# Optimization experiments

Measured on AMD Instinct MI355X. Metric: run time of the kernel, lower is better.

Reference implementation:

```python
import jax, jax.numpy as jnp
import numpy as np
import math

SQRT2 = float(np.sqrt(2.0))
INV_SQRT_2PI = float(1.0 / np.sqrt(2.0 * np.pi))


def _trunc_prob(x, mu, sigma):
    # Faithful port of TruncNormal.prob with a=-10, b=10
    a, b = -10.0, 10.0
    phi_b = 0.5 * (1.0 + jax.scipy.special.erf((b - mu) / sigma / SQRT2))
    phi_a = 0.5 * (1.0 + jax.scipy.special.erf((a - mu) / sigma / SQRT2))
    xs = jnp.where(x > b, x + 100.0, x)
    xs = jnp.where(xs < a, xs - 100.0, xs)
    xn = (xs - mu) / sigma
    dens = jnp.exp(-0.5 * xn * xn) * INV_SQRT_2PI
    dens = jnp.where((xn > b) | (xn < a), 0.0, dens)
    return dens / (phi_b - phi_a) + 1e-10


def _S_single(zg, tt, Wx, bx, Wt, bt, Wt2, bt2, Wf, bf, Wo, bo):
    # One tiny MLP applied to one group-slice zg (shape [g]) at scalar time tt.
    g = Wx.shape[0]
    x = jnp.tanh(Wx @ zg + bx)
    half = g // 2
    freqs = jnp.exp(jnp.arange(half, dtype=zg.dtype) * (-math.log(10000.0) / half))
    te = tt * freqs
    temb = jnp.concatenate([jnp.sin(te), jnp.cos(te)])  # [g]
    tv = jax.nn.gelu(Wt @ temb + bt, approximate=False)  # torch nn.GELU (exact)
    tv = Wt2 @ tv + bt2
    h = jnp.tanh(Wf @ (x + tv) + bf)
    return jnp.tanh(Wo @ h + bo)[0]  # scalar S


def _derivs(zg, tt, Wx, bx, Wt, bt, Wt2, bt2, Wf, bf, Wo, bo):
    p = (Wx, bx, Wt, bt, Wt2, bt2, Wf, bf, Wo, bo)
    f = lambda z_, t_: _S_single(z_, t_, *p)
    S = f(zg, tt)
    s_z = jax.grad(f, 0)(zg, tt)                    # dS/dz         [g]
    H = jax.jacfwd(jax.grad(f, 0), 0)(zg, tt)       # H[j,k]=d2S/dzj dzk  [g,g]
    dSdt = jax.grad(f, 1)(zg, tt)                   # dS/dt scalar
    return S, s_z, H, dSdt


def reference(z, time_step, mu, sigma, Wx, bx, Wt, bt, Wt2, bt2, Wf, bf, Wo, bo, beta):
    G, g = Wx.shape[0], Wx.shape[1]
    B = z.shape[0]
    tt = time_step[0]

    sig2 = sigma ** 2 + 1e-5
    nlp = -(z - mu) / sig2                                   # nabla_log_phi [B,n_in]
    dlp = -1.0 / sig2                                        # delta_log_phi (scalar-ish)
    dpp = ((z - mu) ** 2 - sigma ** 2) / (sigma ** 4 + 1e-5)  # delta_phi_over_phi
    rho = _trunc_prob(z, mu, sigma)

    to_g = lambda a: a.reshape(B, G, g).transpose(1, 0, 2)   # [G,B,g]
    zr, nlp_r, dpp_r, rho_r = to_g(z), to_g(nlp), to_g(dpp), to_g(rho)

    over_b = jax.vmap(_derivs, in_axes=(0, None) + (None,) * 10)
    over_g = jax.vmap(over_b, in_axes=(0, None) + (0,) * 10)
    S, s_z, H, dSdt = over_g(zr, tt, Wx, bx, Wt, bt, Wt2, bt2, Wf, bf, Wo, bo)
    # S [G,B], s_z [G,B,g], H [G,B,g,g], dSdt [G,B]

    bb = beta.reshape(G, 1, 1)
    u = S[..., None] - bb * jnp.log(jnp.prod(rho_r, axis=2, keepdims=True))  # [G,B,1]
    u_z = s_z - bb * nlp_r                                                    # [G,B,g]
    # torch grad(S.sum(), t): t is a single shared (1,1) tensor -> gradient sums over batch
    dSdt_sum = dSdt.sum(axis=1).reshape(G, 1, 1)
    # grad((rho*u_z).sum(), z_temp): rho and nabla_log_phi are constants wrt z_temp,
    # so gradient = sum_j rho_j * H[j,k]
    corr = jnp.einsum('gbj,gbjk->gbk', rho_r, H)
    u_t = dSdt_sum + bb * corr / (rho_r + 1e-5)
    # grad(s_z.sum(), z_temp)[k] = sum_j H[j,k]
    u_zz = H.sum(axis=2) - bb * dlp
    pde = u_t + 0.5 * u_z ** 2 + 0.125 * bb ** 2 * (nlp_r ** 2 - 2.0 * dpp_r)

    to_bn = lambda a: a.transpose(1, 0, 2).reshape(B, -1)
    return to_bn(pde), to_bn(u_z), u[:, :, 0].transpose(1, 0), to_bn(u_zz)


def setup_inputs() -> dict:
    B, N_IN, g = 8192, 512, 4
    G = N_IN // g
    key = jax.random.key(0)
    ks = jax.random.split(key, 16)

    def lin_w(k, fo, fi):
        return (jax.random.normal(k, (G, fo, fi), jnp.float32) / np.sqrt(fi)).astype(jnp.float32)

    def lin_b(k, fo):
        return (0.01 * jax.random.normal(k, (G, fo), jnp.float32)).astype(jnp.float32)

    return {
        "z": jax.random.normal(ks[0], (B, N_IN), jnp.float32),
        "time_step": jnp.ones((1,), jnp.float32),
        "mu": jnp.zeros((1,), jnp.float32),
        "sigma": jnp.ones((1,), jnp.float32),
        "Wx": lin_w(ks[1], g, g), "bx": lin_b(ks[2], g),
        "Wt": lin_w(ks[3], g, g), "bt": lin_b(ks[4], g),
        "Wt2": lin_w(ks[5], g, g), "bt2": lin_b(ks[6], g),
        "Wf": lin_w(ks[7], g, g), "bf": lin_b(ks[8], g),
        "Wo": lin_w(ks[9], 1, g), "bo": lin_b(ks[10], 1),
        "beta": jnp.ones((G, 1), jnp.float32),
    }
```

## Files before the change

### kernel.cpp

```cpp
#include <hip/hip_runtime.h>
#include <math.h>

#define NG 128
#define NIN 512
#define OFF1 4194304
#define OFF2 8388608
#define OFF3 9437184

#define INV_SQRT_2PI 0.3989422804014327f
#define INV_SQRT2    0.7071067811865476f

__device__ __forceinline__ float ftanh(float x){
    float e = __expf(2.0f*x);
    float r = __builtin_amdgcn_rcpf(e + 1.0f);
    return 1.0f - 2.0f*r;
}
__device__ __forceinline__ float frcp(float x){ return __builtin_amdgcn_rcpf(x); }

__device__ __forceinline__ float gelu_f(float x){
    return 0.5f*x*(1.0f + erff(x*INV_SQRT2));
}
__device__ __forceinline__ float gelu_df(float x){
    return 0.5f*(1.0f + erff(x*INV_SQRT2)) + x*INV_SQRT_2PI*expf(-0.5f*x*x);
}

__global__ void k_pre(const float* __restrict__ ts,
                      const float* __restrict__ mup, const float* __restrict__ sigp,
                      const float* __restrict__ Wt,  const float* __restrict__ bt,
                      const float* __restrict__ Wt2, const float* __restrict__ bt2,
                      float* __restrict__ tv_ws, float* __restrict__ dtv_ws,
                      float* __restrict__ consts){
    int g = threadIdx.x;
    if (g == 0){
        float mu = mup[0], sigma = sigp[0];
        float sig2   = sigma*sigma + 1e-5f;
        float phi_b  = 0.5f*(1.0f+erff((10.0f-mu)/sigma*INV_SQRT2));
        float phi_a  = 0.5f*(1.0f+erff((-10.0f-mu)/sigma*INV_SQRT2));
        consts[0] = sig2;
        consts[1] = -1.0f/sig2;
        consts[2] = 1.0f/(sigma*sigma*sigma*sigma + 1e-5f);
        consts[3] = 1.0f/(phi_b-phi_a);
        consts[4] = mu;
        consts[5] = 1.0f/sigma;
        consts[6] = sigma;
    }
    if (g >= NG) return;
    float t  = ts[0];
    float f1 = expf(-0.5f*logf(10000.0f));
    float te0 = t, te1 = t*f1;
    float temb[4]  = { sinf(te0),  sinf(te1),     cosf(te0),     cosf(te1) };
    float dtemb[4] = { cosf(te0),  f1*cosf(te1), -sinf(te0), -f1*sinf(te1) };
    float tg[4], dg[4];
    #pragma unroll
    for (int i=0;i<4;i++){
        float a = bt[g*4+i], d = 0.0f;
        #pragma unroll
        for (int j=0;j<4;j++){
            float w = Wt[g*16+i*4+j];
            a += w*temb[j]; d += w*dtemb[j];
        }
        tg[i] = gelu_f(a);
        dg[i] = gelu_df(a)*d;
    }
    #pragma unroll
    for (int j=0;j<4;j++){
        float a = bt2[g*4+j], d = 0.0f;
        #pragma unroll
        for (int i=0;i<4;i++){
            float w = Wt2[g*16+j*4+i];
            a += w*tg[i]; d += w*dg[i];
        }
        tv_ws[g*4+j]  = a;
        dtv_ws[g*4+j] = d;
    }
}

__global__ __launch_bounds__(256) void k_dsdt(const float* __restrict__ z,
    const float* __restrict__ Wx, const float* __restrict__ bx,
    const float* __restrict__ Wf, const float* __restrict__ bf,
    const float* __restrict__ Wo, const float* __restrict__ bo,
    const float* __restrict__ tv_ws, const float* __restrict__ dtv_ws,
    float* __restrict__ partial){
    const int tid  = threadIdx.x;
    const int gidx = tid & 127;
    const int lb   = tid >> 7;
    float wx[16], wf[16];
    #pragma unroll
    for (int i=0;i<4;i++){
        float4 a4 = ((const float4*)(Wx + gidx*16))[i];
        wx[i*4+0]=a4.x; wx[i*4+1]=a4.y; wx[i*4+2]=a4.z; wx[i*4+3]=a4.w;
        float4 b4 = ((const float4*)(Wf + gidx*16))[i];
        wf[i*4+0]=b4.x; wf[i*4+1]=b4.y; wf[i*4+2]=b4.z; wf[i*4+3]=b4.w;
    }
    float4 t4;
    t4 = ((const float4*)bx)[gidx];     float bxA[4]={t4.x,t4.y,t4.z,t4.w};
    t4 = ((const float4*)bf)[gidx];     float bfA[4]={t4.x,t4.y,t4.z,t4.w};
    t4 = ((const float4*)Wo)[gidx];     float w3[4] ={t4.x,t4.y,t4.z,t4.w};
    t4 = ((const float4*)tv_ws)[gidx];  float tvA[4]={t4.x,t4.y,t4.z,t4.w};
    t4 = ((const float4*)dtv_ws)[gidx]; float dtvA[4]={t4.x,t4.y,t4.z,t4.w};
    float bo0 = bo[gidx];

    float acc = 0.0f;
    const int b0 = blockIdx.x*4 + lb;
    #pragma unroll
    for (int k=0;k<2;k++){
        int b = b0 + 2*k;
        float4 zv = *((const float4*)(z + b*NIN + gidx*4));
        float zz[4]={zv.x,zv.y,zv.z,zv.w};
        float u1[4];
        #pragma unroll
        for (int i=0;i<4;i++){
            float a = bxA[i] + wx[i*4]*zz[0]+wx[i*4+1]*zz[1]+wx[i*4+2]*zz[2]+wx[i*4+3]*zz[3];
            u1[i] = ftanh(a) + tvA[i];
        }
        float hp[4];
        float a3 = bo0;
        #pragma unroll
        for (int i=0;i<4;i++){
            float a = bfA[i] + wf[i*4]*u1[0]+wf[i*4+1]*u1[1]+wf[i*4+2]*u1[2]+wf[i*4+3]*u1[3];
            float h = ftanh(a);
            hp[i] = 1.0f - h*h;
            a3 += w3[i]*h;
        }
        float S = ftanh(a3), sp = 1.0f - S*S;
        float q[4]={0.f,0.f,0.f,0.f};
        #pragma unroll
        for (int i=0;i<4;i++){
            float vi = sp*w3[i]*hp[i];
            #pragma unroll
            for (int j=0;j<4;j++) q[j] += vi*wf[i*4+j];
        }
        acc += q[0]*dtvA[0]+q[1]*dtvA[1]+q[2]*dtvA[2]+q[3]*dtvA[3];
    }
    __shared__ float sred[256];
    sred[tid] = acc;
    __syncthreads();
    if (tid < 128) partial[blockIdx.x*128 + tid] = sred[tid] + sred[tid+128];
}

__global__ __launch_bounds__(256) void k_red(const float* __restrict__ partial,
                                             float* __restrict__ dsum){
    int g = blockIdx.x;
    int tid = threadIdx.x;
    float a = 0.0f;
    for (int i=tid;i<2048;i+=256) a += partial[i*128+g];
    __shared__ float s[256];
    s[tid] = a;
    __syncthreads();
    if (tid < 64){
        a = s[tid] + s[tid+64] + s[tid+128] + s[tid+192];
        #pragma unroll
        for (int o=32;o>0;o>>=1) a += __shfl_down(a, o);
        if (tid==0) dsum[g] = a;
    }
}

__global__ __launch_bounds__(256) void k_main(const float* __restrict__ z,
    const float* __restrict__ Wx, const float* __restrict__ bx,
    const float* __restrict__ Wf, const float* __restrict__ bf,
    const float* __restrict__ Wo, const float* __restrict__ bo,
    const float* __restrict__ betap, const float* __restrict__ tv_ws,
    const float* __restrict__ consts,
    const float* __restrict__ dsum, float* __restrict__ out){
    const int tid  = threadIdx.x;
    const int gidx = tid & 127;
    const int b    = blockIdx.x*2 + (tid>>7);

    const float sig2    = consts[0];
    const float dlp     = consts[1];
    const float inv_s4  = consts[2];
    const float invZ    = consts[3];
    const float mu      = consts[4];
    const float inv_sig = consts[5];
    const float sigma   = consts[6];
    const float inv_sig2 = frcp(sig2);

    float wx[16], wf[16];
    #pragma unroll
    for (int i=0;i<4;i++){
        float4 a4 = ((const float4*)(Wx + gidx*16))[i];
        wx[i*4+0]=a4.x; wx[i*4+1]=a4.y; wx[i*4+2]=a4.z; wx[i*4+3]=a4.w;
        float4 b4 = ((const float4*)(Wf + gidx*16))[i];
        wf[i*4+0]=b4.x; wf[i*4+1]=b4.y; wf[i*4+2]=b4.z; wf[i*4+3]=b4.w;
    }
    float4 t4;
    t4 = ((const float4*)bx)[gidx];    float bxA[4]={t4.x,t4.y,t4.z,t4.w};
    t4 = ((const float4*)bf)[gidx];    float bfA[4]={t4.x,t4.y,t4.z,t4.w};
    t4 = ((const float4*)Wo)[gidx];    float w3[4] ={t4.x,t4.y,t4.z,t4.w};
    t4 = ((const float4*)tv_ws)[gidx]; float tvA[4]={t4.x,t4.y,t4.z,t4.w};
    const float bo0    = bo[gidx];
    const float bb     = betap[gidx];
    const float dS_sum = dsum[gidx];

    float4 zv = *((const float4*)(z + b*NIN + gidx*4));
    float zz[4]={zv.x,zv.y,zv.z,zv.w};

    float x[4], xp[4], u1[4];
    #pragma unroll
    for (int i=0;i<4;i++){
        float a = bxA[i] + wx[i*4]*zz[0]+wx[i*4+1]*zz[1]+wx[i*4+2]*zz[2]+wx[i*4+3]*zz[3];
        x[i] = ftanh(a); xp[i] = 1.0f - x[i]*x[i];
        u1[i] = x[i] + tvA[i];
    }
    float h[4], hp[4];
    float a3 = bo0;
    #pragma unroll
    for (int i=0;i<4;i++){
        float a = bfA[i] + wf[i*4]*u1[0]+wf[i*4+1]*u1[1]+wf[i*4+2]*u1[2]+wf[i*4+3]*u1[3];
        h[i] = ftanh(a); hp[i] = 1.0f - h[i]*h[i];
        a3 += w3[i]*h[i];
    }
    float S = ftanh(a3), sp = 1.0f - S*S;

    float Bm[16];
    #pragma unroll
    for (int i=0;i<4;i++){
        #pragma unroll
        for (int n=0;n<4;n++){
            float s = 0.0f;
            #pragma unroll
            for (int k=0;k<4;k++) s += wf[i*4+k]*xp[k]*wx[k*4+n];
            Bm[i*4+n]=s;
        }
    }
    float w3hp[4], v[4];
    #pragma unroll
    for (int i=0;i<4;i++){ w3hp[i]=w3[i]*hp[i]; v[i]=sp*w3hp[i]; }
    float q[4]={0.f,0.f,0.f,0.f};
    #pragma unroll
    for (int i=0;i<4;i++){
        #pragma unroll
        for (int j=0;j<4;j++) q[j] += v[i]*wf[i*4+j];
    }
    float c[4];
    #pragma unroll
    for (int n=0;n<4;n++){
        float s=0.0f;
        #pragma unroll
        for (int i=0;i<4;i++) s += w3hp[i]*Bm[i*4+n];
        c[n]=s;
    }
    const float alpha = -2.0f*S*sp;
    float bet[4], gam[4];
    #pragma unroll
    for (int i=0;i<4;i++){ bet[i] = -2.0f*h[i]*v[i]; gam[i] = -2.0f*x[i]*xp[i]*q[i]; }

    float rho[4], nlp[4], dpp[4];
    #pragma unroll
    for (int j=0;j<4;j++){
        float zj = zz[j];
        float xs = zj > 10.0f ? zj+100.0f : zj;
        xs = xs < -10.0f ? xs-100.0f : xs;
        float xn = (xs-mu)*inv_sig;
        float dens = __expf(-0.5f*xn*xn)*INV_SQRT_2PI;
        dens = (xn > 10.0f || xn < -10.0f) ? 0.0f : dens;
        rho[j] = dens*invZ + 1e-10f;
        nlp[j] = -(zj-mu)*inv_sig2;
        float d = zj-mu;
        dpp[j] = (d*d - sigma*sigma)*inv_s4;
    }
    float u_val = S - bb*__logf(rho[0]*rho[1]*rho[2]*rho[3]);

    float rc=0.0f, scs=0.0f;
    #pragma unroll
    for (int j=0;j<4;j++){ rc += rho[j]*c[j]; scs += c[j]; }
    float rB[4], sB[4], rA[4], sA[4];
    #pragma unroll
    for (int i=0;i<4;i++){
        float r=0.0f, s=0.0f, r2=0.0f, s2=0.0f;
        #pragma unroll
        for (int j=0;j<4;j++){
            r  += rho[j]*Bm[i*4+j]; s  += Bm[i*4+j];
            r2 += rho[j]*wx[i*4+j]; s2 += wx[i*4+j];
        }
        rB[i]=r; sB[i]=s; rA[i]=r2; sA[i]=s2;
    }

    float pde[4], uz[4], uzz[4];
    #pragma unroll
    for (int k=0;k<4;k++){
        float corr = alpha*rc*c[k];
        float hsum = alpha*scs*c[k];
        #pragma unroll
        for (int i=0;i<4;i++){
            corr += bet[i]*rB[i]*Bm[i*4+k];
            hsum += bet[i]*sB[i]*Bm[i*4+k];
            corr += gam[i]*rA[i]*wx[i*4+k];
            hsum += gam[i]*sA[i]*wx[i*4+k];
        }
        float uzk = sp*c[k] - bb*nlp[k];
        float utk = dS_sum + bb*corr*frcp(rho[k]+1e-5f);
        uz[k]  = uzk;
        uzz[k] = hsum - bb*dlp;
        pde[k] = utk + 0.5f*uzk*uzk + 0.125f*bb*bb*(nlp[k]*nlp[k] - 2.0f*dpp[k]);
    }

    const int base = b*NIN + gidx*4;
    *((float4*)(out + base))        = make_float4(pde[0],pde[1],pde[2],pde[3]);
    *((float4*)(out + OFF1 + base)) = make_float4(uz[0],uz[1],uz[2],uz[3]);
    out[OFF2 + b*NG + gidx] = u_val;
    *((float4*)(out + OFF3 + base)) = make_float4(uzz[0],uzz[1],uzz[2],uzz[3]);
}

extern "C" void kernel_launch(void* const* d_in, const int* in_sizes, int n_in,
                              void* d_out, int out_size, void* d_ws, size_t ws_size,
                              hipStream_t stream){
    (void)in_sizes; (void)n_in; (void)out_size; (void)ws_size;
    const float* z     = (const float*)d_in[0];
    const float* ts    = (const float*)d_in[1];
    const float* mu    = (const float*)d_in[2];
    const float* sigma = (const float*)d_in[3];
    const float* Wx    = (const float*)d_in[4];
    const float* bx    = (const float*)d_in[5];
    const float* Wt    = (const float*)d_in[6];
    const float* bt    = (const float*)d_in[7];
    const float* Wt2   = (const float*)d_in[8];
    const float* bt2   = (const float*)d_in[9];
    const float* Wf    = (const float*)d_in[10];
    const float* bf    = (const float*)d_in[11];
    const float* Wo    = (const float*)d_in[12];
    const float* bo    = (const float*)d_in[13];
    const float* beta  = (const float*)d_in[14];
    float* out = (float*)d_out;

    float* ws      = (float*)d_ws;
    float* tv_ws   = ws;
    float* dtv_ws  = ws + 512;
    float* consts  = ws + 1024;
    float* dsum    = ws + 1032;
    float* partial = ws + 1160;

    k_pre <<<1,   128, 0, stream>>>(ts, mu, sigma, Wt, bt, Wt2, bt2, tv_ws, dtv_ws, consts);
    k_dsdt<<<2048,256, 0, stream>>>(z, Wx, bx, Wf, bf, Wo, bo, tv_ws, dtv_ws, partial);
    k_red <<<128, 256, 0, stream>>>(partial, dsum);
    k_main<<<4096,256, 0, stream>>>(z, Wx, bx, Wf, bf, Wo, bo, beta, tv_ws, consts, dsum, out);
}
```

Baseline: 131.0 us.

## Fuse dS/dt partial sums into main kernel and add deferred pde fixup pass

Merges the time-embedding precompute, the dS/dt partial-reduction kernel and the main derivative kernel into one pass. Each thread now computes the forward pass and derivatives once per row, and the pde output is written without the global dS/dt sum. A small fixup kernel then adds the reduced per-group sum into the pde region. This removes the duplicated forward-pass compute and the second read of z, at the cost of an extra read-modify-write over the pde output and per-block recomputation of the constants and time-embedding MLP.

```diff
diff --git a/kernel.cpp b/kernel.cpp
--- a/kernel.cpp
+++ b/kernel.cpp
@@ -21,69 +21,33 @@
     return 0.5f*x*(1.0f + erff(x*INV_SQRT2));
 }
 __device__ __forceinline__ float gelu_df(float x){
-    return 0.5f*(1.0f + erff(x*INV_SQRT2)) + x*INV_SQRT_2PI*expf(-0.5f*x*x);
-}
-
-__global__ void k_pre(const float* __restrict__ ts,
-                      const float* __restrict__ mup, const float* __restrict__ sigp,
-                      const float* __restrict__ Wt,  const float* __restrict__ bt,
-                      const float* __restrict__ Wt2, const float* __restrict__ bt2,
-                      float* __restrict__ tv_ws, float* __restrict__ dtv_ws,
-                      float* __restrict__ consts){
-    int g = threadIdx.x;
-    if (g == 0){
-        float mu = mup[0], sigma = sigp[0];
-        float sig2   = sigma*sigma + 1e-5f;
-        float phi_b  = 0.5f*(1.0f+erff((10.0f-mu)/sigma*INV_SQRT2));
-        float phi_a  = 0.5f*(1.0f+erff((-10.0f-mu)/sigma*INV_SQRT2));
-        consts[0] = sig2;
-        consts[1] = -1.0f/sig2;
-        consts[2] = 1.0f/(sigma*sigma*sigma*sigma + 1e-5f);
-        consts[3] = 1.0f/(phi_b-phi_a);
-        consts[4] = mu;
-        consts[5] = 1.0f/sigma;
-        consts[6] = sigma;
-    }
-    if (g >= NG) return;
-    float t  = ts[0];
-    float f1 = expf(-0.5f*logf(10000.0f));
-    float te0 = t, te1 = t*f1;
-    float temb[4]  = { sinf(te0),  sinf(te1),     cosf(te0),     cosf(te1) };
-    float dtemb[4] = { cosf(te0),  f1*cosf(te1), -sinf(te0), -f1*sinf(te1) };
-    float tg[4], dg[4];
-    #pragma unroll
-    for (int i=0;i<4;i++){
-        float a = bt[g*4+i], d = 0.0f;
-        #pragma unroll
-        for (int j=0;j<4;j++){
-            float w = Wt[g*16+i*4+j];
-            a += w*temb[j]; d += w*dtemb[j];
-        }
-        tg[i] = gelu_f(a);
-        dg[i] = gelu_df(a)*d;
-    }
-    #pragma unroll
-    for (int j=0;j<4;j++){
-        float a = bt2[g*4+j], d = 0.0f;
-        #pragma unroll
-        for (int i=0;i<4;i++){
-            float w = Wt2[g*16+j*4+i];
-            a += w*tg[i]; d += w*dg[i];
-        }
-        tv_ws[g*4+j]  = a;
-        dtv_ws[g*4+j] = d;
-    }
-}
-
-__global__ __launch_bounds__(256) void k_dsdt(const float* __restrict__ z,
+    return 0.5f*(1.0f + erff(x*INV_SQRT2)) + x*INV_SQRT_2PI*__expf(-0.5f*x*x);
+}
+
+__global__ __launch_bounds__(256) void k_fused(const float* __restrict__ z,
+    const float* __restrict__ ts,
+    const float* __restrict__ mup, const float* __restrict__ sigp,
     const float* __restrict__ Wx, const float* __restrict__ bx,
+    const float* __restrict__ Wt, const float* __restrict__ bt,
+    const float* __restrict__ Wt2, const float* __restrict__ bt2,
     const float* __restrict__ Wf, const float* __restrict__ bf,
     const float* __restrict__ Wo, const float* __restrict__ bo,
-    const float* __restrict__ tv_ws, const float* __restrict__ dtv_ws,
-    float* __restrict__ partial){
+    const float* __restrict__ betap,
+    float* __restrict__ partial, float* __restrict__ out){
     const int tid  = threadIdx.x;
     const int gidx = tid & 127;
     const int lb   = tid >> 7;
+
+    const float mu = mup[0], sigma = sigp[0];
+    const float sig2     = sigma*sigma + 1e-5f;
+    const float inv_sig2 = frcp(sig2);
+    const float dlp      = -inv_sig2;
+    const float inv_s4   = frcp(sigma*sigma*sigma*sigma + 1e-5f);
+    const float inv_sig  = frcp(sigma);
+    const float phi_b    = 0.5f*(1.0f+erff((10.0f-mu)*inv_sig*INV_SQRT2));
+    const float phi_a    = 0.5f*(1.0f+erff((-10.0f-mu)*inv_sig*INV_SQRT2));
+    const float invZ     = frcp(phi_b-phi_a);
+
     float wx[16], wf[16];
     #pragma unroll
     for (int i=0;i<4;i++){
@@ -93,47 +57,166 @@
         wf[i*4+0]=b4.x; wf[i*4+1]=b4.y; wf[i*4+2]=b4.z; wf[i*4+3]=b4.w;
     }
     float4 t4;
-    t4 = ((const float4*)bx)[gidx];     float bxA[4]={t4.x,t4.y,t4.z,t4.w};
-    t4 = ((const float4*)bf)[gidx];     float bfA[4]={t4.x,t4.y,t4.z,t4.w};
-    t4 = ((const float4*)Wo)[gidx];     float w3[4] ={t4.x,t4.y,t4.z,t4.w};
-    t4 = ((const float4*)tv_ws)[gidx];  float tvA[4]={t4.x,t4.y,t4.z,t4.w};
-    t4 = ((const float4*)dtv_ws)[gidx]; float dtvA[4]={t4.x,t4.y,t4.z,t4.w};
-    float bo0 = bo[gidx];
-
-    float acc = 0.0f;
-    const int b0 = blockIdx.x*4 + lb;
-    #pragma unroll
-    for (int k=0;k<2;k++){
-        int b = b0 + 2*k;
+    t4 = ((const float4*)bx)[gidx];    float bxA[4]={t4.x,t4.y,t4.z,t4.w};
+    t4 = ((const float4*)bf)[gidx];    float bfA[4]={t4.x,t4.y,t4.z,t4.w};
+    t4 = ((const float4*)Wo)[gidx];    float w3[4] ={t4.x,t4.y,t4.z,t4.w};
+    const float bo0 = bo[gidx];
+    const float bb  = betap[gidx];
+
+    float tvA[4], dtvA[4];
+    {
+        const float t  = ts[0];
+        const float f1 = 0.01f;
+        float te0 = t, te1 = t*f1;
+        float s0, c0, s1, c1;
+        __sincosf(te0, &s0, &c0);
+        __sincosf(te1, &s1, &c1);
+        float temb[4]  = { s0, s1, c0, c1 };
+        float dtemb[4] = { c0, f1*c1, -s0, -f1*s1 };
+        float tg[4], dg[4];
+        #pragma unroll
+        for (int i=0;i<4;i++){
+            float a = bt[gidx*4+i], d = 0.0f;
+            #pragma unroll
+            for (int j=0;j<4;j++){
+                float w = Wt[gidx*16+i*4+j];
+                a += w*temb[j]; d += w*dtemb[j];
+            }
+            tg[i] = gelu_f(a);
+            dg[i] = gelu_df(a)*d;
+        }
+        #pragma unroll
+        for (int j=0;j<4;j++){
+            float a = bt2[gidx*4+j], d = 0.0f;
+            #pragma unroll
+            for (int i=0;i<4;i++){
+                float w = Wt2[gidx*16+j*4+i];
+                a += w*tg[i]; d += w*dg[i];
+            }
+            tvA[j]  = a;
+            dtvA[j] = d;
+        }
+    }
+
+    float dsdt_acc = 0.0f;
+    const int b_base = blockIdx.x*4 + lb*2;
+
+    for (int r=0;r<2;r++){
+        const int b = b_base + r;
         float4 zv = *((const float4*)(z + b*NIN + gidx*4));
         float zz[4]={zv.x,zv.y,zv.z,zv.w};
-        float u1[4];
+
+        float x[4], xp[4], u1[4];
         #pragma unroll
         for (int i=0;i<4;i++){
             float a = bxA[i] + wx[i*4]*zz[0]+wx[i*4+1]*zz[1]+wx[i*4+2]*zz[2]+wx[i*4+3]*zz[3];
-            u1[i] = ftanh(a) + tvA[i];
-        }
-        float hp[4];
+            x[i] = ftanh(a); xp[i] = 1.0f - x[i]*x[i];
+            u1[i] = x[i] + tvA[i];
+        }
+        float h[4], hp[4];
         float a3 = bo0;
         #pragma unroll
         for (int i=0;i<4;i++){
             float a = bfA[i] + wf[i*4]*u1[0]+wf[i*4+1]*u1[1]+wf[i*4+2]*u1[2]+wf[i*4+3]*u1[3];
-            float h = ftanh(a);
-            hp[i] = 1.0f - h*h;
-            a3 += w3[i]*h;
+            h[i] = ftanh(a); hp[i] = 1.0f - h[i]*h[i];
+            a3 += w3[i]*h[i];
         }
         float S = ftanh(a3), sp = 1.0f - S*S;
+
+        float Bm[16];
+        #pragma unroll
+        for (int i=0;i<4;i++){
+            #pragma unroll
+            for (int n=0;n<4;n++){
+                float s = 0.0f;
+                #pragma unroll
+                for (int k=0;k<4;k++) s += wf[i*4+k]*xp[k]*wx[k*4+n];
+                Bm[i*4+n]=s;
+            }
+        }
+        float w3hp[4], v[4];
+        #pragma unroll
+        for (int i=0;i<4;i++){ w3hp[i]=w3[i]*hp[i]; v[i]=sp*w3hp[i]; }
         float q[4]={0.f,0.f,0.f,0.f};
         #pragma unroll
         for (int i=0;i<4;i++){
-            float vi = sp*w3[i]*hp[i];
-            #pragma unroll
-            for (int j=0;j<4;j++) q[j] += vi*wf[i*4+j];
-        }
-        acc += q[0]*dtvA[0]+q[1]*dtvA[1]+q[2]*dtvA[2]+q[3]*dtvA[3];
-    }
+            #pragma unroll
+            for (int j=0;j<4;j++) q[j] += v[i]*wf[i*4+j];
+        }
+        dsdt_acc += q[0]*dtvA[0]+q[1]*dtvA[1]+q[2]*dtvA[2]+q[3]*dtvA[3];
+
+        float c[4];
+        #pragma unroll
+        for (int n=0;n<4;n++){
+            float s=0.0f;
+            #pragma unroll
+            for (int i=0;i<4;i++) s += w3hp[i]*Bm[i*4+n];
+            c[n]=s;
+        }
+        const float alpha = -2.0f*S*sp;
+        float bet[4], gam[4];
+        #pragma unroll
+        for (int i=0;i<4;i++){ bet[i] = -2.0f*h[i]*v[i]; gam[i] = -2.0f*x[i]*xp[i]*q[i]; }
+
+        float rho[4], nlp[4], dpp[4];
+        #pragma unroll
+        for (int j=0;j<4;j++){
+            float zj = zz[j];
+            float xs = zj > 10.0f ? zj+100.0f : zj;
+            xs = xs < -10.0f ? xs-100.0f : xs;
+            float xn = (xs-mu)*inv_sig;
+            float dens = __expf(-0.5f*xn*xn)*INV_SQRT_2PI;
+            dens = (xn > 10.0f || xn < -10.0f) ? 0.0f : dens;
+            rho[j] = dens*invZ + 1e-10f;
+            nlp[j] = -(zj-mu)*inv_sig2;
+            float d = zj-mu;
+            dpp[j] = (d*d - sigma*sigma)*inv_s4;
+        }
+        float u_val = S - bb*__logf(rho[0]*rho[1]*rho[2]*rho[3]);
+
+        float rc=0.0f, scs=0.0f;
+        #pragma unroll
+        for (int j=0;j<4;j++){ rc += rho[j]*c[j]; scs += c[j]; }
+        float rB[4], sB[4], rA[4], sA[4];
+        #pragma unroll
+        for (int i=0;i<4;i++){
+            float r1=0.0f, s=0.0f, r2=0.0f, s2=0.0f;
+            #pragma unroll
+            for (int j=0;j<4;j++){
+                r1 += rho[j]*Bm[i*4+j]; s  += Bm[i*4+j];
+                r2 += rho[j]*wx[i*4+j]; s2 += wx[i*4+j];
+            }
+            rB[i]=r1; sB[i]=s; rA[i]=r2; sA[i]=s2;
+        }
+
+        float pde[4], uz[4], uzz[4];
+        #pragma unroll
+        for (int k=0;k<4;k++){
+            float corr = alpha*rc*c[k];
+            float hsum = alpha*scs*c[k];
+            #pragma unroll
+            for (int i=0;i<4;i++){
+                corr += bet[i]*rB[i]*Bm[i*4+k];
+                hsum += bet[i]*sB[i]*Bm[i*4+k];
+                corr += gam[i]*rA[i]*wx[i*4+k];
+                hsum += gam[i]*sA[i]*wx[i*4+k];
+            }
+            float uzk = sp*c[k] - bb*nlp[k];
+            uz[k]  = uzk;
+            uzz[k] = hsum - bb*dlp;
+            pde[k] = bb*corr*frcp(rho[k]+1e-5f)
+                   + 0.5f*uzk*uzk + 0.125f*bb*bb*(nlp[k]*nlp[k] - 2.0f*dpp[k]);
+        }
+
+        const int base = b*NIN + gidx*4;
+        *((float4*)(out + base))        = make_float4(pde[0],pde[1],pde[2],pde[3]);
+        *((float4*)(out + OFF1 + base)) = make_float4(uz[0],uz[1],uz[2],uz[3]);
+        out[OFF2 + b*NG + gidx] = u_val;
+        *((float4*)(out + OFF3 + base)) = make_float4(uzz[0],uzz[1],uzz[2],uzz[3]);
+    }
+
     __shared__ float sred[256];
-    sred[tid] = acc;
+    sred[tid] = dsdt_acc;
     __syncthreads();
     if (tid < 128) partial[blockIdx.x*128 + tid] = sred[tid] + sred[tid+128];
 }
@@ -155,151 +238,14 @@
     }
 }
 
-__global__ __launch_bounds__(256) void k_main(const float* __restrict__ z,
-    const float* __restrict__ Wx, const float* __restrict__ bx,
-    const float* __restrict__ Wf, const float* __restrict__ bf,
-    const float* __restrict__ Wo, const float* __restrict__ bo,
-    const float* __restrict__ betap, const float* __restrict__ tv_ws,
-    const float* __restrict__ consts,
-    const float* __restrict__ dsum, float* __restrict__ out){
-    const int tid  = threadIdx.x;
-    const int gidx = tid & 127;
-    const int b    = blockIdx.x*2 + (tid>>7);
-
-    const float sig2    = consts[0];
-    const float dlp     = consts[1];
-    const float inv_s4  = consts[2];
-    const float invZ    = consts[3];
-    const float mu      = consts[4];
-    const float inv_sig = consts[5];
-    const float sigma   = consts[6];
-    const float inv_sig2 = frcp(sig2);
-
-    float wx[16], wf[16];
-    #pragma unroll
-    for (int i=0;i<4;i++){
-        float4 a4 = ((const float4*)(Wx + gidx*16))[i];
-        wx[i*4+0]=a4.x; wx[i*4+1]=a4.y; wx[i*4+2]=a4.z; wx[i*4+3]=a4.w;
-        float4 b4 = ((const float4*)(Wf + gidx*16))[i];
-        wf[i*4+0]=b4.x; wf[i*4+1]=b4.y; wf[i*4+2]=b4.z; wf[i*4+3]=b4.w;
-    }
-    float4 t4;
-    t4 = ((const float4*)bx)[gidx];    float bxA[4]={t4.x,t4.y,t4.z,t4.w};
-    t4 = ((const float4*)bf)[gidx];    float bfA[4]={t4.x,t4.y,t4.z,t4.w};
-    t4 = ((const float4*)Wo)[gidx];    float w3[4] ={t4.x,t4.y,t4.z,t4.w};
-    t4 = ((const float4*)tv_ws)[gidx]; float tvA[4]={t4.x,t4.y,t4.z,t4.w};
-    const float bo0    = bo[gidx];
-    const float bb     = betap[gidx];
-    const float dS_sum = dsum[gidx];
-
-    float4 zv = *((const float4*)(z + b*NIN + gidx*4));
-    float zz[4]={zv.x,zv.y,zv.z,zv.w};
-
-    float x[4], xp[4], u1[4];
-    #pragma unroll
-    for (int i=0;i<4;i++){
-        float a = bxA[i] + wx[i*4]*zz[0]+wx[i*4+1]*zz[1]+wx[i*4+2]*zz[2]+wx[i*4+3]*zz[3];
-        x[i] = ftanh(a); xp[i] = 1.0f - x[i]*x[i];
-        u1[i] = x[i] + tvA[i];
-    }
-    float h[4], hp[4];
-    float a3 = bo0;
-    #pragma unroll
-    for (int i=0;i<4;i++){
-        float a = bfA[i] + wf[i*4]*u1[0]+wf[i*4+1]*u1[1]+wf[i*4+2]*u1[2]+wf[i*4+3]*u1[3];
-        h[i] = ftanh(a); hp[i] = 1.0f - h[i]*h[i];
-        a3 += w3[i]*h[i];
-    }
-    float S = ftanh(a3), sp = 1.0f - S*S;
-
-    float Bm[16];
-    #pragma unroll
-    for (int i=0;i<4;i++){
-        #pragma unroll
-        for (int n=0;n<4;n++){
-            float s = 0.0f;
-            #pragma unroll
-            for (int k=0;k<4;k++) s += wf[i*4+k]*xp[k]*wx[k*4+n];
-            Bm[i*4+n]=s;
-        }
-    }
-    float w3hp[4], v[4];
-    #pragma unroll
-    for (int i=0;i<4;i++){ w3hp[i]=w3[i]*hp[i]; v[i]=sp*w3hp[i]; }
-    float q[4]={0.f,0.f,0.f,0.f};
-    #pragma unroll
-    for (int i=0;i<4;i++){
-        #pragma unroll
-        for (int j=0;j<4;j++) q[j] += v[i]*wf[i*4+j];
-    }
-    float c[4];
-    #pragma unroll
-    for (int n=0;n<4;n++){
-        float s=0.0f;
-        #pragma unroll
-        for (int i=0;i<4;i++) s += w3hp[i]*Bm[i*4+n];
-        c[n]=s;
-    }
-    const float alpha = -2.0f*S*sp;
-    float bet[4], gam[4];
-    #pragma unroll
-    for (int i=0;i<4;i++){ bet[i] = -2.0f*h[i]*v[i]; gam[i] = -2.0f*x[i]*xp[i]*q[i]; }
-
-    float rho[4], nlp[4], dpp[4];
-    #pragma unroll
-    for (int j=0;j<4;j++){
-        float zj = zz[j];
-        float xs = zj > 10.0f ? zj+100.0f : zj;
-        xs = xs < -10.0f ? xs-100.0f : xs;
-        float xn = (xs-mu)*inv_sig;
-        float dens = __expf(-0.5f*xn*xn)*INV_SQRT_2PI;
-        dens = (xn > 10.0f || xn < -10.0f) ? 0.0f : dens;
-        rho[j] = dens*invZ + 1e-10f;
-        nlp[j] = -(zj-mu)*inv_sig2;
-        float d = zj-mu;
-        dpp[j] = (d*d - sigma*sigma)*inv_s4;
-    }
-    float u_val = S - bb*__logf(rho[0]*rho[1]*rho[2]*rho[3]);
-
-    float rc=0.0f, scs=0.0f;
-    #pragma unroll
-    for (int j=0;j<4;j++){ rc += rho[j]*c[j]; scs += c[j]; }
-    float rB[4], sB[4], rA[4], sA[4];
-    #pragma unroll
-    for (int i=0;i<4;i++){
-        float r=0.0f, s=0.0f, r2=0.0f, s2=0.0f;
-        #pragma unroll
-        for (int j=0;j<4;j++){
-            r  += rho[j]*Bm[i*4+j]; s  += Bm[i*4+j];
-            r2 += rho[j]*wx[i*4+j]; s2 += wx[i*4+j];
-        }
-        rB[i]=r; sB[i]=s; rA[i]=r2; sA[i]=s2;
-    }
-
-    float pde[4], uz[4], uzz[4];
-    #pragma unroll
-    for (int k=0;k<4;k++){
-        float corr = alpha*rc*c[k];
-        float hsum = alpha*scs*c[k];
-        #pragma unroll
-        for (int i=0;i<4;i++){
-            corr += bet[i]*rB[i]*Bm[i*4+k];
-            hsum += bet[i]*sB[i]*Bm[i*4+k];
-            corr += gam[i]*rA[i]*wx[i*4+k];
-            hsum += gam[i]*sA[i]*wx[i*4+k];
-        }
-        float uzk = sp*c[k] - bb*nlp[k];
-        float utk = dS_sum + bb*corr*frcp(rho[k]+1e-5f);
-        uz[k]  = uzk;
-        uzz[k] = hsum - bb*dlp;
-        pde[k] = utk + 0.5f*uzk*uzk + 0.125f*bb*bb*(nlp[k]*nlp[k] - 2.0f*dpp[k]);
-    }
-
-    const int base = b*NIN + gidx*4;
-    *((float4*)(out + base))        = make_float4(pde[0],pde[1],pde[2],pde[3]);
-    *((float4*)(out + OFF1 + base)) = make_float4(uz[0],uz[1],uz[2],uz[3]);
-    out[OFF2 + b*NG + gidx] = u_val;
-    *((float4*)(out + OFF3 + base)) = make_float4(uzz[0],uzz[1],uzz[2],uzz[3]);
+__global__ __launch_bounds__(256) void k_fix(const float* __restrict__ dsum,
+                                             float* __restrict__ out){
+    const int idx = blockIdx.x*256 + threadIdx.x;
+    const float ds = dsum[threadIdx.x & 127];
+    float4* p = ((float4*)out) + idx;
+    float4 v = *p;
+    v.x += ds; v.y += ds; v.z += ds; v.w += ds;
+    *p = v;
 }
 
 extern "C" void kernel_launch(void* const* d_in, const int* in_sizes, int n_in,
@@ -324,14 +270,11 @@
     float* out = (float*)d_out;
 
     float* ws      = (float*)d_ws;
-    float* tv_ws   = ws;
-    float* dtv_ws  = ws + 512;
-    float* consts  = ws + 1024;
-    float* dsum    = ws + 1032;
-    float* partial = ws + 1160;
-
-    k_pre <<<1,   128, 0, stream>>>(ts, mu, sigma, Wt, bt, Wt2, bt2, tv_ws, dtv_ws, consts);
-    k_dsdt<<<2048,256, 0, stream>>>(z, Wx, bx, Wf, bf, Wo, bo, tv_ws, dtv_ws, partial);
-    k_red <<<128, 256, 0, stream>>>(partial, dsum);
-    k_main<<<4096,256, 0, stream>>>(z, Wx, bx, Wf, bf, Wo, bo, beta, tv_ws, consts, dsum, out);
-}
+    float* dsum    = ws;
+    float* partial = ws + 128;
+
+    k_fused<<<2048,256, 0, stream>>>(z, ts, mu, sigma, Wx, bx, Wt, bt, Wt2, bt2,
+                                     Wf, bf, Wo, bo, beta, partial, out);
+    k_red  <<<128, 256, 0, stream>>>(partial, dsum);
+    k_fix  <<<4096,256, 0, stream>>>(dsum, out);
+}
```

Result: slower. 138.3 us (+5.5%).
